# Performance work log

Hardware: AMD Instinct MI355X
Metric: run time of the kernel (lower is better)

Reference implementation:

```python
import jax, jax.numpy as jnp
import numpy as np

N, F, C, E = 1024, 64, 4, 32768
H = 256       # MLP hidden width
C_OUT = 4     # new edge channels produced by nn_edge


def setup_inputs() -> dict:
    key = jax.random.key(0)
    ks = jax.random.split(key, 12)
    x = jax.random.normal(ks[0], (N, F), dtype=jnp.float32)
    edge_index = jax.random.randint(ks[1], (C, 2, E), 0, N)
    edge_weight = jax.random.uniform(ks[2], (C, E), dtype=jnp.float32)
    s_n1 = 1.0 / np.sqrt(C * F)
    s_n2 = 1.0 / np.sqrt(H)
    s_e1 = 1.0 / np.sqrt(C + 2 * F)
    return {
        "x": x,
        "edge_index": edge_index,
        "edge_weight": edge_weight,
        "Wn1": jax.random.normal(ks[3], (C * F, H), dtype=jnp.float32) * s_n1,
        "bn1": jnp.zeros((H,), jnp.float32),
        "Wn2": jax.random.normal(ks[4], (H, F), dtype=jnp.float32) * s_n2,
        "bn2": jnp.zeros((F,), jnp.float32),
        "We1": jax.random.normal(ks[5], (C + 2 * F, H), dtype=jnp.float32) * s_e1,
        "be1": jnp.zeros((H,), jnp.float32),
        "We2": jax.random.normal(ks[6], (H, C_OUT), dtype=jnp.float32) * s_n2,
        "be2": jnp.zeros((C_OUT,), jnp.float32),
        "eps": jnp.zeros((), jnp.float32),
    }


def reference(x, edge_index, edge_weight, Wn1, bn1, Wn2, bn2, We1, be1, We2, be2, eps):
    # ---- MCGNN: per-channel edge-weighted scatter-add aggregation ----
    def agg_one(ei, w):
        # ei: [2,E] (row0 = source j, row1 = target i); w: [E]
        msg = x[ei[0]] * w[:, None]                       # [E,F]
        return jax.ops.segment_sum(msg, ei[1], num_segments=N)  # [N,F]

    agg = jax.vmap(agg_one)(edge_index, edge_weight)      # [C,N,F]
    out_cat = agg + (1.0 + eps) * x                       # broadcast self term
    h = out_cat.transpose(1, 0, 2).reshape(N, C * F)      # [N, C*F]
    x_next = jax.nn.relu(h @ Wn1 + bn1) @ Wn2 + bn2       # [N,F]

    # ---- EDPGNN: dense adjacency per channel + broadcast x_i/x_j ----
    def dense_adj(ei, w):
        return jnp.zeros((N, N), x.dtype).at[ei[0], ei[1]].add(w)

    a = jax.vmap(dense_adj)(edge_index, edge_weight)      # [C,N,N]
    a = a.transpose(1, 2, 0)                              # [N,N,C]
    x_i = jnp.broadcast_to(x_next[:, None, :], (N, N, F))
    x_j = jnp.broadcast_to(x_next[None, :, :], (N, N, F))
    feat = jnp.concatenate([a, x_i, x_j], axis=2).reshape(N * N, C + 2 * F)
    adj_out = (jax.nn.relu(feat @ We1 + be1) @ We2 + be2).reshape(N, N, C_OUT)
    return adj_out
```

## Files before the change

### kernel.cpp

```cpp
#include <hip/hip_runtime.h>

#define NN 1024
#define FF 64
#define CC 4
#define EE 32768
#define HH 256

#define OFF_ADENSE 0u
#define OFF_CNT    4194304u
#define OFF_MASK   4198400u
#define OFF_OFFS   4231168u
#define OFF_CURSOR 4235268u
#define OFF_SRTS   4239364u
#define OFF_SRTW   4370436u
#define OFF_P      4501508u
#define OFF_Q      4763652u
#define OFF_QT     5025796u

__global__ __launch_bounds__(256)
void k_count(const int* __restrict__ ei, int* __restrict__ cnt,
             float4* __restrict__ adense4)
{
    unsigned t = blockIdx.x * 256u + threadIdx.x;
    unsigned e = t & (EE - 1u);
    unsigned c = t >> 15;
    int dst = ei[c * 2 * EE + EE + e];
    atomicAdd(&cnt[c * NN + dst], 1);

    const unsigned base = blockIdx.x * 2048u + threadIdx.x;
    const float4 z = make_float4(0.f, 0.f, 0.f, 0.f);
#pragma unroll
    for (int u = 0; u < 8; ++u)
        adense4[base + u * 256u] = z;
}

__global__ __launch_bounds__(256)
void k_scan(const int* __restrict__ cnt, int* __restrict__ offs, int* __restrict__ cursor)
{
    __shared__ int wsum[4];
    const int t = threadIdx.x;
    int c[16];
    int s = 0;
    const int4* cp = (const int4*)(cnt + t * 16);
#pragma unroll
    for (int u = 0; u < 4; ++u) {
        int4 v = cp[u];
        c[u * 4 + 0] = v.x; c[u * 4 + 1] = v.y; c[u * 4 + 2] = v.z; c[u * 4 + 3] = v.w;
        s += v.x + v.y + v.z + v.w;
    }
    int incl = s;
#pragma unroll
    for (int d = 1; d < 64; d <<= 1) {
        int v = __shfl_up(incl, d, 64);
        if ((t & 63) >= d) incl += v;
    }
    const int w = t >> 6;
    if ((t & 63) == 63) wsum[w] = incl;
    __syncthreads();
    int base = incl - s;
    for (int ww = 0; ww < w; ++ww) base += wsum[ww];
    int run = base;
#pragma unroll
    for (int u = 0; u < 16; ++u) {
        offs[t * 16 + u] = run;
        cursor[t * 16 + u] = run;
        run += c[u];
    }
    if (t == 255) offs[4096] = run;
}

__global__ __launch_bounds__(256)
void k_bucket_adj(const int* __restrict__ ei, const float* __restrict__ ew,
                  int* __restrict__ cursor, int* __restrict__ srt_src,
                  float* __restrict__ srt_w, float* __restrict__ adense,
                  unsigned* __restrict__ mask)
{
    unsigned t = blockIdx.x * 256u + threadIdx.x;
    unsigned e = t & (EE - 1u);
    unsigned c = t >> 15;
    int src = ei[c * 2 * EE + e];
    int dst = ei[c * 2 * EE + EE + e];
    float w = ew[c * EE + e];
    int pos = atomicAdd(&cursor[c * NN + dst], 1);
    srt_src[pos] = src;
    srt_w[pos] = w;
    unsigned pair = (unsigned)src * NN + (unsigned)dst;
    atomicAdd(&adense[(size_t)pair * CC + c], w);
    atomicOr(&mask[pair >> 5], 1u << (pair & 31u));
}

__global__ __launch_bounds__(1024)
void k_node(const float* __restrict__ x, const int* __restrict__ offs,
            const int* __restrict__ srt_src, const float* __restrict__ srt_w,
            const float* __restrict__ Wn1, const float* __restrict__ bn1,
            const float* __restrict__ Wn2, const float* __restrict__ bn2,
            const float* __restrict__ We1, const float* __restrict__ be1,
            const float* __restrict__ epsp,
            float* __restrict__ P, float* __restrict__ Q)
{
    __shared__ float hval[4][256];
    __shared__ float hidl[4][256];
    __shared__ float part[4][4][64];
    __shared__ float xnl[4][64];
    const int tid = threadIdx.x;
    const int n0 = blockIdx.x * 4;

    {
        const int w = tid >> 6, lane = tid & 63;
        const int c = w & 3, nn = w >> 2;
        const int g = c * NN + (n0 + nn);
        const int beg = offs[g], end = offs[g + 1];
        float acc = 0.f;
        for (int k = beg; k < end; ++k)
            acc += x[srt_src[k] * FF + lane] * srt_w[k];
        const float ope = 1.0f + epsp[0];
        hval[nn][c * 64 + lane] = acc + ope * x[(n0 + nn) * FF + lane];
    }
    __syncthreads();

    {
        const int nn = tid >> 8, h = tid & 255;
        float acc = bn1[h];
#pragma unroll 8
        for (int k = 0; k < 256; ++k)
            acc += hval[nn][k] * Wn1[k * 256 + h];
        hidl[nn][h] = fmaxf(acc, 0.f);
    }
    __syncthreads();

    {
        const int kq = tid >> 8, nn = (tid >> 6) & 3, f = tid & 63;
        float p = 0.f;
#pragma unroll 8
        for (int k = kq * 64; k < kq * 64 + 64; ++k)
            p += hidl[nn][k] * Wn2[k * 64 + f];
        part[kq][nn][f] = p;
    }
    __syncthreads();
    if (tid < 256) {
        const int nn = tid >> 6, f = tid & 63;
        xnl[nn][f] = bn2[f] + part[0][nn][f] + part[1][nn][f]
                             + part[2][nn][f] + part[3][nn][f];
    }
    __syncthreads();

    {
        const int r = tid >> 8, h = tid & 255;
        float p = be1[h], q = 0.f;
#pragma unroll 8
        for (int f = 0; f < 64; ++f) {
            float xv = xnl[r][f];
            p += xv * We1[(4 + f) * 256 + h];
            q += xv * We1[(68 + f) * 256 + h];
        }
        P[(n0 + r) * 256 + h] = p;
        Q[(n0 + r) * 256 + h] = q;
    }
}

__global__ __launch_bounds__(256)
void k_qt(const float4* __restrict__ Q4, float4* __restrict__ QTP)
{
    __shared__ float4 qt[32 * 64];
    const int t = threadIdx.x;
    const int n0 = blockIdx.x * 32;
#pragma unroll
    for (int u = 0; u < 8; ++u) {
        int idx = t + u * 256;
        int row = idx >> 6, quad = idx & 63;
        qt[row * 64 + (quad ^ (row & 7))] = Q4[(n0 + row) * 64 + quad];
    }
    __syncthreads();
#pragma unroll
    for (int u = 0; u < 8; ++u) {
        int idx = t + u * 256;
        int hq = idx >> 5, jl = idx & 31;
        QTP[hq * NN + n0 + jl] = qt[jl * 64 + (hq ^ (jl & 7))];
    }
}

__global__ __launch_bounds__(256, 4)
void k_edge_mlp(const float* __restrict__ P, const float* __restrict__ Q,
                const float4* __restrict__ QTP, const float* __restrict__ adense,
                const unsigned* __restrict__ mask, const float* __restrict__ We1,
                const float* __restrict__ We2, const float* __restrict__ be2,
                float* __restrict__ out)
{
    __shared__ float4 delta[256];
    __shared__ int nzlist[256];
    __shared__ int lcnt;

    const int tid = threadIdx.x;
    const int w = tid >> 6, lane = tid & 63;
    const int iBase = blockIdx.y * 4, jBase = blockIdx.x * 64;
    const int i = __builtin_amdgcn_readfirstlane(iBase + w);
    const int j = jBase + lane;

    if (tid == 0) lcnt = 0;
    __syncthreads();

    const unsigned mw = mask[(unsigned)i * 32u + ((unsigned)j >> 5)];
    const bool nz = (mw >> (j & 31)) & 1u;
    if (nz) { int idx = atomicAdd(&lcnt, 1); nzlist[idx] = tid; }

    const float4* P4  = (const float4*)P;
    const float4* W24 = (const float4*)We2;
    float ax = 0.f, ay = 0.f, az = 0.f, aw = 0.f;
    for (int hq = 0; hq < 64; ++hq) {
        const float4 qv  = QTP[hq * NN + j];
        const float4 pv  = P4[(size_t)i * 64 + hq];
        const float4 w20 = W24[hq * 4 + 0];
        const float4 w21 = W24[hq * 4 + 1];
        const float4 w22 = W24[hq * 4 + 2];
        const float4 w23 = W24[hq * 4 + 3];
        const float v0 = fmaxf(pv.x + qv.x, 0.f);
        const float v1 = fmaxf(pv.y + qv.y, 0.f);
        const float v2 = fmaxf(pv.z + qv.z, 0.f);
        const float v3 = fmaxf(pv.w + qv.w, 0.f);
        ax += v0 * w20.x + v1 * w21.x + v2 * w22.x + v3 * w23.x;
        ay += v0 * w20.y + v1 * w21.y + v2 * w22.y + v3 * w23.y;
        az += v0 * w20.z + v1 * w21.z + v2 * w22.z + v3 * w23.z;
        aw += v0 * w20.w + v1 * w21.w + v2 * w22.w + v3 * w23.w;
    }

    __syncthreads();
    {
        const int nfix = lcnt;
        for (int pi = w; pi < nfix; pi += 4) {
            const int lij = nzlist[pi];
            const int gi = iBase + (lij >> 6), gj = jBase + (lij & 63);
            const float4 a = *(const float4*)(adense + ((size_t)gi * NN + gj) * 4);
            float o0 = 0.f, o1 = 0.f, o2 = 0.f, o3 = 0.f;
#pragma unroll
            for (int u = 0; u < 4; ++u) {
                const int h = u * 64 + lane;
                float s = a.x * We1[0 * 256 + h] + a.y * We1[1 * 256 + h]
                        + a.z * We1[2 * 256 + h] + a.w * We1[3 * 256 + h];
                float v = fmaxf(P[gi * 256 + h] + Q[gj * 256 + h] + s, 0.f);
                const float4 w2 = W24[h];
                o0 += v * w2.x; o1 += v * w2.y; o2 += v * w2.z; o3 += v * w2.w;
            }
#pragma unroll
            for (int d = 32; d > 0; d >>= 1) {
                o0 += __shfl_down(o0, d, 64);
                o1 += __shfl_down(o1, d, 64);
                o2 += __shfl_down(o2, d, 64);
                o3 += __shfl_down(o3, d, 64);
            }
            if (lane == 0)
                delta[lij] = make_float4(o0, o1, o2, o3);
        }
    }
    __syncthreads();

    const float4 b2 = *(const float4*)be2;
    const float4 dfx = delta[tid];
    float4 o;
    o.x = (nz ? dfx.x : ax) + b2.x;
    o.y = (nz ? dfx.y : ay) + b2.y;
    o.z = (nz ? dfx.z : az) + b2.z;
    o.w = (nz ? dfx.w : aw) + b2.w;
    *(float4*)(out + ((size_t)i * NN + j) * 4) = o;
}

extern "C" void kernel_launch(void* const* d_in, const int* in_sizes, int n_in,
                              void* d_out, int out_size, void* d_ws, size_t ws_size,
                              hipStream_t stream)
{
    (void)in_sizes; (void)n_in; (void)out_size; (void)ws_size;
    const float* x   = (const float*)d_in[0];
    const int*   ei  = (const int*)d_in[1];
    const float* ew  = (const float*)d_in[2];
    const float* Wn1 = (const float*)d_in[3];
    const float* bn1 = (const float*)d_in[4];
    const float* Wn2 = (const float*)d_in[5];
    const float* bn2 = (const float*)d_in[6];
    const float* We1 = (const float*)d_in[7];
    const float* be1 = (const float*)d_in[8];
    const float* We2 = (const float*)d_in[9];
    const float* be2 = (const float*)d_in[10];
    const float* eps = (const float*)d_in[11];
    float* out = (float*)d_out;

    float*    ws     = (float*)d_ws;
    float*    adense = ws + OFF_ADENSE;
    int*      cnt    = (int*)(ws + OFF_CNT);
    unsigned* mask   = (unsigned*)(ws + OFF_MASK);
    int*      offs   = (int*)(ws + OFF_OFFS);
    int*      cursor = (int*)(ws + OFF_CURSOR);
    int*      srts   = (int*)(ws + OFF_SRTS);
    float*    srtw   = ws + OFF_SRTW;
    float*    Pb     = ws + OFF_P;
    float*    Qb     = ws + OFF_Q;
    float*    QTb    = ws + OFF_QT;

    (void)hipMemsetAsync((void*)cnt, 0, (size_t)(4096 + 32768) * sizeof(int), stream);

    k_count     <<<(CC * EE) / 256, 256, 0, stream>>>(ei, cnt, (float4*)adense);
    k_scan      <<<1, 256, 0, stream>>>(cnt, offs, cursor);
    k_bucket_adj<<<(CC * EE) / 256, 256, 0, stream>>>(ei, ew, cursor, srts, srtw,
                                                      adense, mask);
    k_node      <<<NN / 4, 1024, 0, stream>>>(x, offs, srts, srtw,
                                              Wn1, bn1, Wn2, bn2, We1, be1, eps, Pb, Qb);
    k_qt        <<<NN / 32, 256, 0, stream>>>((const float4*)Qb, (float4*)QTb);

    dim3 g(NN / 64, NN / 4);
    k_edge_mlp<<<g, 256, 0, stream>>>(Pb, Qb, (const float4*)QTb, adense, mask,
                                      We1, We2, be2, out);
}
```

Measured before the change: 225.0 us.

## Register-block four rows per wave in edge MLP and shrink transpose tiles

Each wave in the edge MLP kernel now computes four output rows instead of one. Each QTP and We2 load is reused across four i rows, and the grid shrinks by a factor of four in y. The transpose kernel uses 8-row tiles with a different swizzle, so it launches more, smaller blocks. The cost is more registers (four float4 accumulators), larger shared arrays, and fewer blocks, which may lower occupancy or parallelism.

```diff
diff --git a/kernel.cpp b/kernel.cpp
--- a/kernel.cpp
+++ b/kernel.cpp
@@ -161,21 +161,21 @@
 __global__ __launch_bounds__(256)
 void k_qt(const float4* __restrict__ Q4, float4* __restrict__ QTP)
 {
-    __shared__ float4 qt[32 * 64];
+    __shared__ float4 qt[8 * 64];
     const int t = threadIdx.x;
-    const int n0 = blockIdx.x * 32;
-#pragma unroll
-    for (int u = 0; u < 8; ++u) {
+    const int n0 = blockIdx.x * 8;
+#pragma unroll
+    for (int u = 0; u < 2; ++u) {
         int idx = t + u * 256;
         int row = idx >> 6, quad = idx & 63;
-        qt[row * 64 + (quad ^ (row & 7))] = Q4[(n0 + row) * 64 + quad];
-    }
-    __syncthreads();
-#pragma unroll
-    for (int u = 0; u < 8; ++u) {
+        qt[row * 64 + (quad ^ (row << 3))] = Q4[(n0 + row) * 64 + quad];
+    }
+    __syncthreads();
+#pragma unroll
+    for (int u = 0; u < 2; ++u) {
         int idx = t + u * 256;
-        int hq = idx >> 5, jl = idx & 31;
-        QTP[hq * NN + n0 + jl] = qt[jl * 64 + (hq ^ (jl & 7))];
+        int hq = idx >> 3, jl = idx & 7;
+        QTP[hq * NN + n0 + jl] = qt[jl * 64 + (hq ^ (jl << 3))];
     }
 }
 
@@ -186,44 +186,58 @@
                 const float* __restrict__ We2, const float* __restrict__ be2,
                 float* __restrict__ out)
 {
-    __shared__ float4 delta[256];
-    __shared__ int nzlist[256];
+    __shared__ float4 delta[1024];
+    __shared__ int nzlist[1024];
     __shared__ int lcnt;
 
     const int tid = threadIdx.x;
     const int w = tid >> 6, lane = tid & 63;
-    const int iBase = blockIdx.y * 4, jBase = blockIdx.x * 64;
-    const int i = __builtin_amdgcn_readfirstlane(iBase + w);
+    const int iBase = blockIdx.y * 16, jBase = blockIdx.x * 64;
     const int j = jBase + lane;
+    const int i0 = __builtin_amdgcn_readfirstlane(iBase + w * 4);
 
     if (tid == 0) lcnt = 0;
     __syncthreads();
 
-    const unsigned mw = mask[(unsigned)i * 32u + ((unsigned)j >> 5)];
-    const bool nz = (mw >> (j & 31)) & 1u;
-    if (nz) { int idx = atomicAdd(&lcnt, 1); nzlist[idx] = tid; }
+    unsigned nzbits = 0;
+#pragma unroll
+    for (int ii = 0; ii < 4; ++ii) {
+        const unsigned mw = mask[(unsigned)(i0 + ii) * 32u + ((unsigned)j >> 5)];
+        if ((mw >> (j & 31)) & 1u) {
+            nzbits |= 1u << ii;
+            int idx = atomicAdd(&lcnt, 1);
+            nzlist[idx] = (w * 4 + ii) * 64 + lane;
+        }
+    }
+    __syncthreads();
 
     const float4* P4  = (const float4*)P;
     const float4* W24 = (const float4*)We2;
-    float ax = 0.f, ay = 0.f, az = 0.f, aw = 0.f;
+
+    float4 acc[4];
+#pragma unroll
+    for (int ii = 0; ii < 4; ++ii) acc[ii] = make_float4(0.f, 0.f, 0.f, 0.f);
+
     for (int hq = 0; hq < 64; ++hq) {
         const float4 qv  = QTP[hq * NN + j];
-        const float4 pv  = P4[(size_t)i * 64 + hq];
         const float4 w20 = W24[hq * 4 + 0];
         const float4 w21 = W24[hq * 4 + 1];
         const float4 w22 = W24[hq * 4 + 2];
         const float4 w23 = W24[hq * 4 + 3];
-        const float v0 = fmaxf(pv.x + qv.x, 0.f);
-        const float v1 = fmaxf(pv.y + qv.y, 0.f);
-        const float v2 = fmaxf(pv.z + qv.z, 0.f);
-        const float v3 = fmaxf(pv.w + qv.w, 0.f);
-        ax += v0 * w20.x + v1 * w21.x + v2 * w22.x + v3 * w23.x;
-        ay += v0 * w20.y + v1 * w21.y + v2 * w22.y + v3 * w23.y;
-        az += v0 * w20.z + v1 * w21.z + v2 * w22.z + v3 * w23.z;
-        aw += v0 * w20.w + v1 * w21.w + v2 * w22.w + v3 * w23.w;
-    }
-
-    __syncthreads();
+#pragma unroll
+        for (int ii = 0; ii < 4; ++ii) {
+            const float4 pv = P4[(size_t)(i0 + ii) * 64 + hq];
+            const float v0 = fmaxf(pv.x + qv.x, 0.f);
+            const float v1 = fmaxf(pv.y + qv.y, 0.f);
+            const float v2 = fmaxf(pv.z + qv.z, 0.f);
+            const float v3 = fmaxf(pv.w + qv.w, 0.f);
+            acc[ii].x += v0 * w20.x + v1 * w21.x + v2 * w22.x + v3 * w23.x;
+            acc[ii].y += v0 * w20.y + v1 * w21.y + v2 * w22.y + v3 * w23.y;
+            acc[ii].z += v0 * w20.z + v1 * w21.z + v2 * w22.z + v3 * w23.z;
+            acc[ii].w += v0 * w20.w + v1 * w21.w + v2 * w22.w + v3 * w23.w;
+        }
+    }
+
     {
         const int nfix = lcnt;
         for (int pi = w; pi < nfix; pi += 4) {
@@ -254,13 +268,18 @@
     __syncthreads();
 
     const float4 b2 = *(const float4*)be2;
-    const float4 dfx = delta[tid];
-    float4 o;
-    o.x = (nz ? dfx.x : ax) + b2.x;
-    o.y = (nz ? dfx.y : ay) + b2.y;
-    o.z = (nz ? dfx.z : az) + b2.z;
-    o.w = (nz ? dfx.w : aw) + b2.w;
-    *(float4*)(out + ((size_t)i * NN + j) * 4) = o;
+#pragma unroll
+    for (int ii = 0; ii < 4; ++ii) {
+        const int lij = (w * 4 + ii) * 64 + lane;
+        const float4 dfx = delta[lij];
+        const bool nzf = (nzbits >> ii) & 1u;
+        float4 o;
+        o.x = (nzf ? dfx.x : acc[ii].x) + b2.x;
+        o.y = (nzf ? dfx.y : acc[ii].y) + b2.y;
+        o.z = (nzf ? dfx.z : acc[ii].z) + b2.z;
+        o.w = (nzf ? dfx.w : acc[ii].w) + b2.w;
+        *(float4*)(out + ((size_t)(i0 + ii) * NN + j) * 4) = o;
+    }
 }
 
 extern "C" void kernel_launch(void* const* d_in, const int* in_sizes, int n_in,
@@ -302,9 +321,9 @@
                                                       adense, mask);
     k_node      <<<NN / 4, 1024, 0, stream>>>(x, offs, srts, srtw,
                                               Wn1, bn1, Wn2, bn2, We1, be1, eps, Pb, Qb);
-    k_qt        <<<NN / 32, 256, 0, stream>>>((const float4*)Qb, (float4*)QTb);
-
-    dim3 g(NN / 64, NN / 4);
+    k_qt        <<<NN / 8, 256, 0, stream>>>((const float4*)Qb, (float4*)QTb);
+
+    dim3 g(NN / 64, NN / 16);
     k_edge_mlp<<<g, 256, 0, stream>>>(Pb, Qb, (const float4*)QTb, adense, mask,
                                       We1, We2, be2, out);
 }
```

Result: slower. 231.6 us (+2.9%).
